# Optimization experiments

Hardware: AMD Instinct MI355X
Metric: run time of the kernel (lower is better)

Reference implementation:

```python
import jax, jax.numpy as jnp
import numpy as np

B = 8192
D1 = 1024
D2 = 1024
H = 4096  # subnet hidden width
SCALE_LIMIT = 1.0


def _mlp(x, W1, b1, W2, b2):
    # Linear -> ReLU -> Linear
    return jnp.maximum(x @ W1 + b1, 0.0) @ W2 + b2


def setup_inputs() -> dict:
    key = jax.random.key(0)
    ks = jax.random.split(key, 17)
    inp = {"x": jax.random.normal(ks[0], (B, D1 + D2), dtype=jnp.float32)}
    # four subnets: s1,t1 map d2->d1 ; s2,t2 map d1->d2
    specs = {"s1": (D2, D1), "t1": (D2, D1), "s2": (D1, D2), "t2": (D1, D2)}
    i = 1
    for name, (din, dout) in specs.items():
        inp[f"{name}_W1"] = 0.02 * jax.random.normal(ks[i], (din, H), dtype=jnp.float32); i += 1
        inp[f"{name}_b1"] = jnp.zeros((H,), dtype=jnp.float32)
        inp[f"{name}_W2"] = 0.02 * jax.random.normal(ks[i], (H, dout), dtype=jnp.float32); i += 1
        inp[f"{name}_b2"] = jnp.zeros((dout,), dtype=jnp.float32)
    return inp


def reference(x,
              s1_W1, s1_b1, s1_W2, s1_b2,
              t1_W1, t1_b1, t1_W2, t1_b2,
              s2_W1, s2_b1, s2_W2, s2_b2,
              t2_W1, t2_b1, t2_W2, t2_b2):
    x1, x2 = x[:, :D1], x[:, D1:]
    # first half-step: update x1 conditioned on x2
    s2v = jnp.tanh(_mlp(x2, s1_W1, s1_b1, s1_W2, s1_b2)) * SCALE_LIMIT  # [B, D1]
    t2v = _mlp(x2, t1_W1, t1_b1, t1_W2, t1_b2)                          # [B, D1]
    y1 = x1 * jnp.exp(s2v) + t2v
    # second half-step: update x2 conditioned on y1
    s1v = jnp.tanh(_mlp(y1, s2_W1, s2_b1, s2_W2, s2_b2)) * SCALE_LIMIT  # [B, D2]
    t1v = _mlp(y1, t2_W1, t2_b1, t2_W2, t2_b2)                          # [B, D2]
    y2 = x2 * jnp.exp(s1v) + t1v
    y = jnp.concatenate([y1, y2], axis=1)  # [B, D1+D2]
    # exact triangular-coupling log-det (what the autograd loop computes per-sample)
    log_det = jnp.sum(s2v, axis=1) + jnp.sum(s1v, axis=1)  # [B]
    return y, log_det
```

## Files before the change

### kernel.cpp

```cpp
#include <hip/hip_runtime.h>
#include <hip/hip_bf16.h>
#include <cstdint>
#include <cstddef>

#define BDIM 8192
#define D1 1024
#define D2 1024
#define HDIM 4096

#define BM 128
#define BN 128
#define BK 64

typedef __attribute__((ext_vector_type(8))) short short8;
typedef __attribute__((ext_vector_type(4))) float f32x4;

__device__ inline void async_load16(const void* g, void* l) {
  __builtin_amdgcn_global_load_lds(
      (const __attribute__((address_space(1))) void*)g,
      (__attribute__((address_space(3))) void*)l,
      16 , 0 , 0 );
}

__device__ inline unsigned short f2bf(float f) {
  union { float f; uint32_t u; } v; v.f = f;
  uint32_t u = v.u;
  uint32_t r = u + 0x7FFFu + ((u >> 16) & 1u);
  return (unsigned short)(r >> 16);
}

__global__ __launch_bounds__(256, 2)
void gemm_bt(const unsigned short* __restrict__ A0,
             const unsigned short* __restrict__ A1,
             const unsigned short* __restrict__ B0,
             const unsigned short* __restrict__ B1,
             const float* __restrict__ bias0,
             const float* __restrict__ bias1,
             void* __restrict__ C0v, void* __restrict__ C1v,
             int M, int N, int K, int mode) {
  const unsigned short* A = blockIdx.z ? A1 : A0;
  const unsigned short* B = blockIdx.z ? B1 : B0;
  const float* bias = blockIdx.z ? bias1 : bias0;

  __shared__ __align__(16) unsigned short lsA[BM * BK];
  __shared__ __align__(16) unsigned short lsB[BN * BK];

  const int tid  = threadIdx.x;
  const int wave = tid >> 6;
  const int lane = tid & 63;
  const int quad = lane >> 4;
  const int l15  = lane & 15;

  const int m0 = blockIdx.y * BM;
  const int n0 = blockIdx.x * BN;
  const int wrow = (wave >> 1) * 64;
  const int wcol = (wave & 1) * 64;

  f32x4 acc[4][4] = {};

  for (int k0 = 0; k0 < K; k0 += BK) {
    __syncthreads();
#pragma unroll
    for (int i = 0; i < 4; ++i) {
      int s   = (wave * 4 + i) * 64 + lane;
      int row = s >> 3;
      int kg  = (s & 7) ^ (row & 7);
      const unsigned short* ga = A + (long)(m0 + row) * K + k0 + kg * 8;
      async_load16(ga, &lsA[(wave * 4 + i) * 512]);
      const unsigned short* gb = B + (long)(n0 + row) * K + k0 + kg * 8;
      async_load16(gb, &lsB[(wave * 4 + i) * 512]);
    }
    __syncthreads();

#pragma unroll
    for (int ks = 0; ks < 2; ++ks) {
      short8 af[4], bfr[4];
      const int kg = ks * 4 + quad;
#pragma unroll
      for (int t = 0; t < 4; ++t) {
        int row = wrow + t * 16 + l15;
        int pa  = row * 8 + (kg ^ (row & 7));
        af[t] = *(const short8*)&lsA[pa * 8];
        int col = wcol + t * 16 + l15;
        int pb  = col * 8 + (kg ^ (col & 7));
        bfr[t] = *(const short8*)&lsB[pb * 8];
      }
#pragma unroll
      for (int mt = 0; mt < 4; ++mt)
#pragma unroll
        for (int nt = 0; nt < 4; ++nt)
          acc[mt][nt] = __builtin_amdgcn_mfma_f32_16x16x32_bf16(
              af[mt], bfr[nt], acc[mt][nt], 0, 0, 0);
    }
  }

  if (mode == 0) {
    unsigned short* C = blockIdx.z ? (unsigned short*)C1v : (unsigned short*)C0v;
#pragma unroll
    for (int mt = 0; mt < 4; ++mt)
#pragma unroll
      for (int nt = 0; nt < 4; ++nt) {
        int col = n0 + wcol + nt * 16 + l15;
        float bv = bias[col];
#pragma unroll
        for (int r = 0; r < 4; ++r) {
          int row = m0 + wrow + mt * 16 + quad * 4 + r;
          float v = acc[mt][nt][r] + bv;
          v = v > 0.f ? v : 0.f;
          C[(long)row * N + col] = f2bf(v);
        }
      }
  } else {
    float* C = blockIdx.z ? (float*)C1v : (float*)C0v;
#pragma unroll
    for (int mt = 0; mt < 4; ++mt)
#pragma unroll
      for (int nt = 0; nt < 4; ++nt) {
        int col = n0 + wcol + nt * 16 + l15;
        float bv = bias[col];
#pragma unroll
        for (int r = 0; r < 4; ++r) {
          int row = m0 + wrow + mt * 16 + quad * 4 + r;
          C[(long)row * N + col] = acc[mt][nt][r] + bv;
        }
      }
  }
}

__global__ __launch_bounds__(256)
void transpose_cast(const float* __restrict__ in, unsigned short* __restrict__ out,
                    int R, int C) {
  __shared__ float tile[32][33];
  const int bx = blockIdx.x * 32;
  const int by = blockIdx.y * 32;
  const int tx = threadIdx.x & 31;
  const int ty = threadIdx.x >> 5;
  for (int j = ty; j < 32; j += 8)
    tile[j][tx] = in[(long)(by + j) * C + bx + tx];
  __syncthreads();
  for (int j = ty; j < 32; j += 8)
    out[(long)(bx + j) * R + by + tx] = f2bf(tile[tx][j]);
}

__global__ __launch_bounds__(256)
void cast_x2(const float* __restrict__ x, unsigned short* __restrict__ x2b) {
  long i = (long)blockIdx.x * 256 + threadIdx.x;
  long row = i >> 10, col = i & 1023;
  x2b[i] = f2bf(x[row * (D1 + D2) + D2 + col]);
}

__global__ __launch_bounds__(256)
void coupling(const float* __restrict__ s_lin, const float* __restrict__ t_lin,
              const float* __restrict__ x, float* __restrict__ y_out,
              unsigned short* __restrict__ y_bf, float* __restrict__ ld_partial,
              float* __restrict__ ld_out, int stage, int moff) {
  const int r = blockIdx.x;
  const long g = moff + r;
  const int tid = threadIdx.x;
  const int off = stage ? D1 : 0;
  float part = 0.f;
  for (int c = tid; c < D1; c += 256) {
    float sv = tanhf(s_lin[(long)r * D1 + c]);
    part += sv;
    float y = x[g * (D1 + D2) + off + c] * expf(sv) + t_lin[(long)r * D1 + c];
    y_out[g * (D1 + D2) + off + c] = y;
    if (y_bf) y_bf[g * D1 + c] = f2bf(y);
  }
  for (int o = 32; o > 0; o >>= 1) part += __shfl_down(part, o, 64);
  __shared__ float red[4];
  if ((tid & 63) == 0) red[tid >> 6] = part;
  __syncthreads();
  if (tid == 0) {
    float tot = red[0] + red[1] + red[2] + red[3];
    if (stage == 0) ld_partial[g] = tot;
    else            ld_out[g] = ld_partial[g] + tot;
  }
}

extern "C" void kernel_launch(void* const* d_in, const int* in_sizes, int n_in,
                              void* d_out, int out_size, void* d_ws, size_t ws_size,
                              hipStream_t stream) {
  const float* x     = (const float*)d_in[0];
  const float* s1_W1 = (const float*)d_in[1];
  const float* s1_b1 = (const float*)d_in[2];
  const float* s1_W2 = (const float*)d_in[3];
  const float* s1_b2 = (const float*)d_in[4];
  const float* t1_W1 = (const float*)d_in[5];
  const float* t1_b1 = (const float*)d_in[6];
  const float* t1_W2 = (const float*)d_in[7];
  const float* t1_b2 = (const float*)d_in[8];
  const float* s2_W1 = (const float*)d_in[9];
  const float* s2_b1 = (const float*)d_in[10];
  const float* s2_W2 = (const float*)d_in[11];
  const float* s2_b2 = (const float*)d_in[12];
  const float* t2_W1 = (const float*)d_in[13];
  const float* t2_b1 = (const float*)d_in[14];
  const float* t2_W2 = (const float*)d_in[15];
  const float* t2_b2 = (const float*)d_in[16];

  const size_t MB = 1024UL * 1024UL;
  int NC = 32;
  {
    const int cand[6] = {1, 2, 4, 8, 16, 32};
    for (int i = 0; i < 6; ++i) {
      size_t need = 81 * MB + (192 * MB) / (size_t)cand[i];
      if (need <= ws_size) { NC = cand[i]; break; }
    }
  }
  const int Mrows = BDIM / NC;

  char* ws = (char*)d_ws;
  float* ldp = (float*)(ws + 0);
  unsigned short* w1t[4], * w2t[4];
  for (int i = 0; i < 4; ++i) {
    w1t[i] = (unsigned short*)(ws + (1 + 8 * (size_t)i) * MB);
    w2t[i] = (unsigned short*)(ws + (33 + 8 * (size_t)i) * MB);
  }
  unsigned short* xyb = (unsigned short*)(ws + 65 * MB);
  size_t hbytes = (size_t)Mrows * HDIM * 2;
  size_t sbytes = (size_t)Mrows * D1 * 4;
  unsigned short* h_s = (unsigned short*)(ws + 81 * MB);
  unsigned short* h_t = (unsigned short*)(ws + 81 * MB + hbytes);
  float* slin = (float*)(ws + 81 * MB + 2 * hbytes);
  float* tlin = (float*)(ws + 81 * MB + 2 * hbytes + sbytes);

  float* y_out  = (float*)d_out;
  float* ld_out = (float*)d_out + (long)BDIM * (D1 + D2);

  cast_x2<<<(BDIM * D1) / 256, 256, 0, stream>>>(x, xyb);
  transpose_cast<<<dim3(HDIM / 32, D1 / 32), 256, 0, stream>>>(s1_W1, w1t[0], D1, HDIM);
  transpose_cast<<<dim3(HDIM / 32, D1 / 32), 256, 0, stream>>>(t1_W1, w1t[1], D1, HDIM);
  transpose_cast<<<dim3(HDIM / 32, D1 / 32), 256, 0, stream>>>(s2_W1, w1t[2], D1, HDIM);
  transpose_cast<<<dim3(HDIM / 32, D1 / 32), 256, 0, stream>>>(t2_W1, w1t[3], D1, HDIM);
  transpose_cast<<<dim3(D1 / 32, HDIM / 32), 256, 0, stream>>>(s1_W2, w2t[0], HDIM, D1);
  transpose_cast<<<dim3(D1 / 32, HDIM / 32), 256, 0, stream>>>(t1_W2, w2t[1], HDIM, D1);
  transpose_cast<<<dim3(D1 / 32, HDIM / 32), 256, 0, stream>>>(s2_W2, w2t[2], HDIM, D1);
  transpose_cast<<<dim3(D1 / 32, HDIM / 32), 256, 0, stream>>>(t2_W2, w2t[3], HDIM, D1);

  for (int c = 0; c < NC; ++c) {
    const int moff = c * Mrows;
    const unsigned short* xA = xyb + (size_t)moff * D1;

    gemm_bt<<<dim3(HDIM / BN, Mrows / BM, 2), 256, 0, stream>>>(
        xA, xA, w1t[0], w1t[1], s1_b1, t1_b1, h_s, h_t, Mrows, HDIM, D1, 0);
    gemm_bt<<<dim3(D1 / BN, Mrows / BM, 2), 256, 0, stream>>>(
        h_s, h_t, w2t[0], w2t[1], s1_b2, t1_b2, slin, tlin, Mrows, D1, HDIM, 1);
    coupling<<<Mrows, 256, 0, stream>>>(slin, tlin, x, y_out, xyb, ldp, nullptr, 0, moff);

    const unsigned short* yA = xyb + (size_t)moff * D1;
    gemm_bt<<<dim3(HDIM / BN, Mrows / BM, 2), 256, 0, stream>>>(
        yA, yA, w1t[2], w1t[3], s2_b1, t2_b1, h_s, h_t, Mrows, HDIM, D1, 0);
    gemm_bt<<<dim3(D1 / BN, Mrows / BM, 2), 256, 0, stream>>>(
        h_s, h_t, w2t[2], w2t[3], s2_b2, t2_b2, slin, tlin, Mrows, D1, HDIM, 1);
    coupling<<<Mrows, 256, 0, stream>>>(slin, tlin, x, y_out, nullptr, ldp, ld_out, 1, moff);
  }
}
```

Before: 932.1 us.

## Fuse s/t subnet GEMMs and fold coupling into the second GEMM epilogue

The first-layer GEMM now computes the s and t subnets in one block, loading the shared activation tile once and keeping two accumulator sets. The second-layer GEMM computes both subnets together and applies tanh, exp, the affine coupling, the bf16 cast of y and the log-det row sums directly in its epilogue. The log-det is accumulated with shared and global atomics after a zero-init kernel. This removes the fp32 slin/tlin intermediates, the separate coupling kernels and redundant A-tile loads. In exchange it doubles accumulator registers and LDS per block, which may reduce occupancy, and makes the log-det summation order depend on atomic timing.

```diff
diff --git a/kernel.cpp b/kernel.cpp
--- a/kernel.cpp
+++ b/kernel.cpp
@@ -5,7 +5,6 @@
 
 #define BDIM 8192
 #define D1 1024
-#define D2 1024
 #define HDIM 4096
 
 #define BM 128
@@ -30,33 +29,30 @@
 }
 
 __global__ __launch_bounds__(256, 2)
-void gemm_bt(const unsigned short* __restrict__ A0,
-             const unsigned short* __restrict__ A1,
-             const unsigned short* __restrict__ B0,
-             const unsigned short* __restrict__ B1,
-             const float* __restrict__ bias0,
-             const float* __restrict__ bias1,
-             void* __restrict__ C0v, void* __restrict__ C1v,
-             int M, int N, int K, int mode) {
-  const unsigned short* A = blockIdx.z ? A1 : A0;
-  const unsigned short* B = blockIdx.z ? B1 : B0;
-  const float* bias = blockIdx.z ? bias1 : bias0;
-
+void gemm1_fused(const unsigned short* __restrict__ A,
+                 const unsigned short* __restrict__ Bs,
+                 const unsigned short* __restrict__ Bt,
+                 const float* __restrict__ bias_s,
+                 const float* __restrict__ bias_t,
+                 unsigned short* __restrict__ Cs,
+                 unsigned short* __restrict__ Ct) {
+  const int K = 1024, N = 4096;
   __shared__ __align__(16) unsigned short lsA[BM * BK];
-  __shared__ __align__(16) unsigned short lsB[BN * BK];
+  __shared__ __align__(16) unsigned short lsS[BN * BK];
+  __shared__ __align__(16) unsigned short lsT[BN * BK];
 
   const int tid  = threadIdx.x;
   const int wave = tid >> 6;
   const int lane = tid & 63;
   const int quad = lane >> 4;
   const int l15  = lane & 15;
-
   const int m0 = blockIdx.y * BM;
   const int n0 = blockIdx.x * BN;
   const int wrow = (wave >> 1) * 64;
   const int wcol = (wave & 1) * 64;
 
-  f32x4 acc[4][4] = {};
+  f32x4 accS[4][4] = {};
+  f32x4 accT[4][4] = {};
 
   for (int k0 = 0; k0 < K; k0 += BK) {
     __syncthreads();
@@ -65,66 +61,161 @@
       int s   = (wave * 4 + i) * 64 + lane;
       int row = s >> 3;
       int kg  = (s & 7) ^ (row & 7);
-      const unsigned short* ga = A + (long)(m0 + row) * K + k0 + kg * 8;
-      async_load16(ga, &lsA[(wave * 4 + i) * 512]);
-      const unsigned short* gb = B + (long)(n0 + row) * K + k0 + kg * 8;
-      async_load16(gb, &lsB[(wave * 4 + i) * 512]);
+      async_load16(A  + (long)(m0 + row) * K + k0 + kg * 8, &lsA[(wave * 4 + i) * 512]);
+      async_load16(Bs + (long)(n0 + row) * K + k0 + kg * 8, &lsS[(wave * 4 + i) * 512]);
+      async_load16(Bt + (long)(n0 + row) * K + k0 + kg * 8, &lsT[(wave * 4 + i) * 512]);
     }
     __syncthreads();
 
 #pragma unroll
     for (int ks = 0; ks < 2; ++ks) {
-      short8 af[4], bfr[4];
+      short8 af[4], bs[4], bt[4];
+      const int kg = ks * 4 + quad;
+#pragma unroll
+      for (int t = 0; t < 4; ++t) {
+        int row = wrow + t * 16 + l15;
+        af[t] = *(const short8*)&lsA[(row * 8 + (kg ^ (row & 7))) * 8];
+        int col = wcol + t * 16 + l15;
+        int pb  = col * 8 + (kg ^ (col & 7));
+        bs[t] = *(const short8*)&lsS[pb * 8];
+        bt[t] = *(const short8*)&lsT[pb * 8];
+      }
+#pragma unroll
+      for (int mt = 0; mt < 4; ++mt)
+#pragma unroll
+        for (int nt = 0; nt < 4; ++nt) {
+          accS[mt][nt] = __builtin_amdgcn_mfma_f32_16x16x32_bf16(
+              af[mt], bs[nt], accS[mt][nt], 0, 0, 0);
+          accT[mt][nt] = __builtin_amdgcn_mfma_f32_16x16x32_bf16(
+              af[mt], bt[nt], accT[mt][nt], 0, 0, 0);
+        }
+    }
+  }
+
+#pragma unroll
+  for (int nt = 0; nt < 4; ++nt) {
+    int col = n0 + wcol + nt * 16 + l15;
+    float bvs = bias_s[col], bvt = bias_t[col];
+#pragma unroll
+    for (int mt = 0; mt < 4; ++mt)
+#pragma unroll
+      for (int r = 0; r < 4; ++r) {
+        long row = m0 + wrow + mt * 16 + quad * 4 + r;
+        float vs = accS[mt][nt][r] + bvs;
+        float vt = accT[mt][nt][r] + bvt;
+        Cs[row * N + col] = f2bf(vs > 0.f ? vs : 0.f);
+        Ct[row * N + col] = f2bf(vt > 0.f ? vt : 0.f);
+      }
+  }
+}
+
+__global__ __launch_bounds__(256, 2)
+void gemm2_fused(const unsigned short* __restrict__ As,
+                 const unsigned short* __restrict__ At,
+                 const unsigned short* __restrict__ Bs,
+                 const unsigned short* __restrict__ Bt,
+                 const float* __restrict__ bias_s,
+                 const float* __restrict__ bias_t,
+                 const float* __restrict__ x,
+                 float* __restrict__ y_out,
+                 unsigned short* __restrict__ y_bf,
+                 float* __restrict__ ld_out,
+                 int moff, int stage) {
+  const int K = 4096;
+  __shared__ __align__(16) unsigned short lsAs[BM * BK];
+  __shared__ __align__(16) unsigned short lsAt[BM * BK];
+  __shared__ __align__(16) unsigned short lsS[BN * BK];
+  __shared__ __align__(16) unsigned short lsT[BN * BK];
+  __shared__ float rowsum[BM];
+
+  const int tid  = threadIdx.x;
+  const int wave = tid >> 6;
+  const int lane = tid & 63;
+  const int quad = lane >> 4;
+  const int l15  = lane & 15;
+  const int m0 = blockIdx.y * BM;
+  const int n0 = blockIdx.x * BN;
+  const int wrow = (wave >> 1) * 64;
+  const int wcol = (wave & 1) * 64;
+
+  f32x4 accS[4][4] = {};
+  f32x4 accT[4][4] = {};
+
+  for (int k0 = 0; k0 < K; k0 += BK) {
+    __syncthreads();
+#pragma unroll
+    for (int i = 0; i < 4; ++i) {
+      int s   = (wave * 4 + i) * 64 + lane;
+      int row = s >> 3;
+      int kg  = (s & 7) ^ (row & 7);
+      long go = (long)row * K + k0 + kg * 8;
+      async_load16(As + (long)m0 * K + go, &lsAs[(wave * 4 + i) * 512]);
+      async_load16(At + (long)m0 * K + go, &lsAt[(wave * 4 + i) * 512]);
+      async_load16(Bs + (long)n0 * K + go, &lsS[(wave * 4 + i) * 512]);
+      async_load16(Bt + (long)n0 * K + go, &lsT[(wave * 4 + i) * 512]);
+    }
+    __syncthreads();
+
+#pragma unroll
+    for (int ks = 0; ks < 2; ++ks) {
+      short8 as[4], at[4], bs[4], bt[4];
       const int kg = ks * 4 + quad;
 #pragma unroll
       for (int t = 0; t < 4; ++t) {
         int row = wrow + t * 16 + l15;
         int pa  = row * 8 + (kg ^ (row & 7));
-        af[t] = *(const short8*)&lsA[pa * 8];
+        as[t] = *(const short8*)&lsAs[pa * 8];
+        at[t] = *(const short8*)&lsAt[pa * 8];
         int col = wcol + t * 16 + l15;
         int pb  = col * 8 + (kg ^ (col & 7));
-        bfr[t] = *(const short8*)&lsB[pb * 8];
+        bs[t] = *(const short8*)&lsS[pb * 8];
+        bt[t] = *(const short8*)&lsT[pb * 8];
       }
 #pragma unroll
       for (int mt = 0; mt < 4; ++mt)
 #pragma unroll
-        for (int nt = 0; nt < 4; ++nt)
-          acc[mt][nt] = __builtin_amdgcn_mfma_f32_16x16x32_bf16(
-              af[mt], bfr[nt], acc[mt][nt], 0, 0, 0);
-    }
-  }
-
-  if (mode == 0) {
-    unsigned short* C = blockIdx.z ? (unsigned short*)C1v : (unsigned short*)C0v;
-#pragma unroll
-    for (int mt = 0; mt < 4; ++mt)
+        for (int nt = 0; nt < 4; ++nt) {
+          accS[mt][nt] = __builtin_amdgcn_mfma_f32_16x16x32_bf16(
+              as[mt], bs[nt], accS[mt][nt], 0, 0, 0);
+          accT[mt][nt] = __builtin_amdgcn_mfma_f32_16x16x32_bf16(
+              at[mt], bt[nt], accT[mt][nt], 0, 0, 0);
+        }
+    }
+  }
+
+  if (tid < BM) rowsum[tid] = 0.f;
+  __syncthreads();
+
+  const int off = stage ? D1 : 0;
+  float bvs[4], bvt[4];
+#pragma unroll
+  for (int nt = 0; nt < 4; ++nt) {
+    int col = n0 + wcol + nt * 16 + l15;
+    bvs[nt] = bias_s[col];
+    bvt[nt] = bias_t[col];
+  }
+#pragma unroll
+  for (int mt = 0; mt < 4; ++mt)
+#pragma unroll
+    for (int r = 0; r < 4; ++r) {
+      long grow = (long)moff + m0 + wrow + mt * 16 + quad * 4 + r;
+      float rs = 0.f;
 #pragma unroll
       for (int nt = 0; nt < 4; ++nt) {
         int col = n0 + wcol + nt * 16 + l15;
-        float bv = bias[col];
-#pragma unroll
-        for (int r = 0; r < 4; ++r) {
-          int row = m0 + wrow + mt * 16 + quad * 4 + r;
-          float v = acc[mt][nt][r] + bv;
-          v = v > 0.f ? v : 0.f;
-          C[(long)row * N + col] = f2bf(v);
-        }
+        float sv = tanhf(accS[mt][nt][r] + bvs[nt]);
+        rs += sv;
+        float t  = accT[mt][nt][r] + bvt[nt];
+        float y  = x[grow * (2 * D1) + off + col] * __expf(sv) + t;
+        y_out[grow * (2 * D1) + off + col] = y;
+        if (y_bf) y_bf[grow * D1 + col] = f2bf(y);
       }
-  } else {
-    float* C = blockIdx.z ? (float*)C1v : (float*)C0v;
-#pragma unroll
-    for (int mt = 0; mt < 4; ++mt)
-#pragma unroll
-      for (int nt = 0; nt < 4; ++nt) {
-        int col = n0 + wcol + nt * 16 + l15;
-        float bv = bias[col];
-#pragma unroll
-        for (int r = 0; r < 4; ++r) {
-          int row = m0 + wrow + mt * 16 + quad * 4 + r;
-          C[(long)row * N + col] = acc[mt][nt][r] + bv;
-        }
-      }
-  }
+#pragma unroll
+      for (int o = 8; o > 0; o >>= 1) rs += __shfl_down(rs, o, 16);
+      if (l15 == 0) atomicAdd(&rowsum[wrow + mt * 16 + quad * 4 + r], rs);
+    }
+  __syncthreads();
+  if (tid < BM) atomicAdd(&ld_out[moff + m0 + tid], rowsum[tid]);
 }
 
 __global__ __launch_bounds__(256)
@@ -146,35 +237,13 @@
 void cast_x2(const float* __restrict__ x, unsigned short* __restrict__ x2b) {
   long i = (long)blockIdx.x * 256 + threadIdx.x;
   long row = i >> 10, col = i & 1023;
-  x2b[i] = f2bf(x[row * (D1 + D2) + D2 + col]);
+  x2b[i] = f2bf(x[row * (2 * D1) + D1 + col]);
 }
 
 __global__ __launch_bounds__(256)
-void coupling(const float* __restrict__ s_lin, const float* __restrict__ t_lin,
-              const float* __restrict__ x, float* __restrict__ y_out,
-              unsigned short* __restrict__ y_bf, float* __restrict__ ld_partial,
-              float* __restrict__ ld_out, int stage, int moff) {
-  const int r = blockIdx.x;
-  const long g = moff + r;
-  const int tid = threadIdx.x;
-  const int off = stage ? D1 : 0;
-  float part = 0.f;
-  for (int c = tid; c < D1; c += 256) {
-    float sv = tanhf(s_lin[(long)r * D1 + c]);
-    part += sv;
-    float y = x[g * (D1 + D2) + off + c] * expf(sv) + t_lin[(long)r * D1 + c];
-    y_out[g * (D1 + D2) + off + c] = y;
-    if (y_bf) y_bf[g * D1 + c] = f2bf(y);
-  }
-  for (int o = 32; o > 0; o >>= 1) part += __shfl_down(part, o, 64);
-  __shared__ float red[4];
-  if ((tid & 63) == 0) red[tid >> 6] = part;
-  __syncthreads();
-  if (tid == 0) {
-    float tot = red[0] + red[1] + red[2] + red[3];
-    if (stage == 0) ld_partial[g] = tot;
-    else            ld_out[g] = ld_partial[g] + tot;
-  }
+void zero_f(float* __restrict__ p, int n) {
+  int i = blockIdx.x * 256 + threadIdx.x;
+  if (i < n) p[i] = 0.f;
 }
 
 extern "C" void kernel_launch(void* const* d_in, const int* in_sizes, int n_in,
@@ -203,30 +272,27 @@
   {
     const int cand[6] = {1, 2, 4, 8, 16, 32};
     for (int i = 0; i < 6; ++i) {
-      size_t need = 81 * MB + (192 * MB) / (size_t)cand[i];
+      size_t need = 80 * MB + (128 * MB) / (size_t)cand[i];
       if (need <= ws_size) { NC = cand[i]; break; }
     }
   }
   const int Mrows = BDIM / NC;
 
   char* ws = (char*)d_ws;
-  float* ldp = (float*)(ws + 0);
   unsigned short* w1t[4], * w2t[4];
   for (int i = 0; i < 4; ++i) {
-    w1t[i] = (unsigned short*)(ws + (1 + 8 * (size_t)i) * MB);
-    w2t[i] = (unsigned short*)(ws + (33 + 8 * (size_t)i) * MB);
-  }
-  unsigned short* xyb = (unsigned short*)(ws + 65 * MB);
+    w1t[i] = (unsigned short*)(ws + (8 * (size_t)i) * MB);
+    w2t[i] = (unsigned short*)(ws + (32 + 8 * (size_t)i) * MB);
+  }
+  unsigned short* xyb = (unsigned short*)(ws + 64 * MB);
   size_t hbytes = (size_t)Mrows * HDIM * 2;
-  size_t sbytes = (size_t)Mrows * D1 * 4;
-  unsigned short* h_s = (unsigned short*)(ws + 81 * MB);
-  unsigned short* h_t = (unsigned short*)(ws + 81 * MB + hbytes);
-  float* slin = (float*)(ws + 81 * MB + 2 * hbytes);
-  float* tlin = (float*)(ws + 81 * MB + 2 * hbytes + sbytes);
+  unsigned short* h_s = (unsigned short*)(ws + 80 * MB);
+  unsigned short* h_t = (unsigned short*)(ws + 80 * MB + hbytes);
 
   float* y_out  = (float*)d_out;
-  float* ld_out = (float*)d_out + (long)BDIM * (D1 + D2);
-
+  float* ld_out = (float*)d_out + (long)BDIM * (2 * D1);
+
+  zero_f<<<(BDIM + 255) / 256, 256, 0, stream>>>(ld_out, BDIM);
   cast_x2<<<(BDIM * D1) / 256, 256, 0, stream>>>(x, xyb);
   transpose_cast<<<dim3(HDIM / 32, D1 / 32), 256, 0, stream>>>(s1_W1, w1t[0], D1, HDIM);
   transpose_cast<<<dim3(HDIM / 32, D1 / 32), 256, 0, stream>>>(t1_W1, w1t[1], D1, HDIM);
@@ -239,19 +305,16 @@
 
   for (int c = 0; c < NC; ++c) {
     const int moff = c * Mrows;
-    const unsigned short* xA = xyb + (size_t)moff * D1;
-
-    gemm_bt<<<dim3(HDIM / BN, Mrows / BM, 2), 256, 0, stream>>>(
-        xA, xA, w1t[0], w1t[1], s1_b1, t1_b1, h_s, h_t, Mrows, HDIM, D1, 0);
-    gemm_bt<<<dim3(D1 / BN, Mrows / BM, 2), 256, 0, stream>>>(
-        h_s, h_t, w2t[0], w2t[1], s1_b2, t1_b2, slin, tlin, Mrows, D1, HDIM, 1);
-    coupling<<<Mrows, 256, 0, stream>>>(slin, tlin, x, y_out, xyb, ldp, nullptr, 0, moff);
-
-    const unsigned short* yA = xyb + (size_t)moff * D1;
-    gemm_bt<<<dim3(HDIM / BN, Mrows / BM, 2), 256, 0, stream>>>(
-        yA, yA, w1t[2], w1t[3], s2_b1, t2_b1, h_s, h_t, Mrows, HDIM, D1, 0);
-    gemm_bt<<<dim3(D1 / BN, Mrows / BM, 2), 256, 0, stream>>>(
-        h_s, h_t, w2t[2], w2t[3], s2_b2, t2_b2, slin, tlin, Mrows, D1, HDIM, 1);
-    coupling<<<Mrows, 256, 0, stream>>>(slin, tlin, x, y_out, nullptr, ldp, ld_out, 1, moff);
-  }
-}
+    unsigned short* xA = xyb + (size_t)moff * D1;
+
+    gemm1_fused<<<dim3(HDIM / BN, Mrows / BM), 256, 0, stream>>>(
+        xA, w1t[0], w1t[1], s1_b1, t1_b1, h_s, h_t);
+    gemm2_fused<<<dim3(D1 / BN, Mrows / BM), 256, 0, stream>>>(
+        h_s, h_t, w2t[0], w2t[1], s1_b2, t1_b2, x, y_out, xyb, ld_out, moff, 0);
+
+    gemm1_fused<<<dim3(HDIM / BN, Mrows / BM), 256, 0, stream>>>(
+        xA, w1t[2], w1t[3], s2_b1, t2_b1, h_s, h_t);
+    gemm2_fused<<<dim3(D1 / BN, Mrows / BM), 256, 0, stream>>>(
+        h_s, h_t, w2t[2], w2t[3], s2_b2, t2_b2, x, y_out, nullptr, ld_out, moff, 1);
+  }
+}
```

Result: faster. 913.2 us (-2.0%).
